# Kernel optimization log

Hardware: AMD Instinct MI355X
Metric: run time of the kernel (lower is better)

Reference implementation:

```python
import jax, jax.numpy as jnp
import numpy as np

B, D, H = 4096, 1024, 1024


def setup_inputs() -> dict:
    key = jax.random.key(0)
    ks = jax.random.split(key, 20)
    s_in = 1.0 / np.sqrt(D)
    s_hid = 1.0 / np.sqrt(H)
    inp = {
        "x_t": jax.random.normal(ks[0], (B, D), dtype=jnp.float32),
        "h_t_1": jax.random.normal(ks[1], (B, H), dtype=jnp.float32),
        "c_t_1": jax.random.normal(ks[2], (B, H), dtype=jnp.float32),
        # input-to-hidden weights (nn.Linear: y = x @ W.T + b), stacked i,f,o,z
        "W": jax.random.uniform(ks[3], (4, H, D), minval=-s_in, maxval=s_in, dtype=jnp.float32),
        "bW": jax.random.uniform(ks[4], (4, H), minval=-s_in, maxval=s_in, dtype=jnp.float32),
        # hidden-to-hidden weights, stacked i,f,o,z
        "U": jax.random.uniform(ks[5], (4, H, H), minval=-s_hid, maxval=s_hid, dtype=jnp.float32),
        "bU": jax.random.uniform(ks[6], (4, H), minval=-s_hid, maxval=s_hid, dtype=jnp.float32),
    }
    return inp


def reference(x_t, h_t_1, c_t_1, W, bW, U, bU):
    # Two stacked GEMMs: [B,D]x[4,H,D] -> [4,B,H], [B,H]x[4,H,H] -> [4,B,H]
    gx = jnp.einsum("bd,ghd->gbh", x_t, W) + bW[:, None, :]
    gh = jnp.einsum("bh,gkh->gbk", h_t_1, U) + bU[:, None, :]
    g = gx + gh  # [4, B, H] pre-activations for i, f, o, z
    i = jax.nn.sigmoid(g[0])
    f = jax.nn.sigmoid(g[1])
    o = jax.nn.sigmoid(g[2])
    z = jnp.tanh(g[3])
    c_t = i * z + f * c_t_1
    h_t = o * jnp.tanh(c_t)
    return (h_t, c_t)
```

## Files before the change

kernel.cpp:

```cpp
#include <hip/hip_runtime.h>
#include <math.h>

#define Mm 4096
#define Nn 4096
#define Kk 2048

typedef __bf16 bf16x8 __attribute__((ext_vector_type(8)));
typedef float f32x4 __attribute__((ext_vector_type(4)));

__device__ __forceinline__ unsigned short f2bf(float f) {
    union { float f; unsigned u; } v; v.f = f;
    unsigned r = v.u + 0x7FFFu + ((v.u >> 16) & 1u);
    return (unsigned short)(r >> 16);
}

__global__ void pack_bf16(const float* __restrict__ x, const float* __restrict__ h,
                          const float* __restrict__ W, const float* __restrict__ U,
                          const float* __restrict__ bW, const float* __restrict__ bU,
                          unsigned short* __restrict__ Xc, unsigned short* __restrict__ Wc,
                          float* __restrict__ bsum) {
    if (blockIdx.x == 0) {
#pragma unroll
        for (int j = 0; j < 16; ++j) {
            int n = threadIdx.x * 16 + j;
            int hh = n >> 2, g = n & 3;
            bsum[n] = bW[g * 1024 + hh] + bU[g * 1024 + hh];
        }
    }
    const int PER = (4096 * 1024) / 4;
    for (int t = blockIdx.x * blockDim.x + threadIdx.x; t < 4 * PER;
         t += gridDim.x * blockDim.x) {
        int region = t >> 20;
        int i = t & (PER - 1);
        int row = i >> 8;
        int c4  = i & 255;
        const float* src = (region == 0) ? x : (region == 1) ? h : (region == 2) ? W : U;
        float4 v = reinterpret_cast<const float4*>(src)[i];
        ushort4 o;
        o.x = f2bf(v.x); o.y = f2bf(v.y); o.z = f2bf(v.z); o.w = f2bf(v.w);
        if (region < 2) {
            *reinterpret_cast<ushort4*>(Xc + (size_t)row * 2048 + (region << 10) + c4 * 4) = o;
        } else {
            int g = row >> 10, hh = row & 1023;
            *reinterpret_cast<ushort4*>(Wc + (size_t)(hh * 4 + g) * 2048 + ((region & 1) << 10) + c4 * 4) = o;
        }
    }
}

__device__ __forceinline__ void gl16(const void* g, void* l) {
    __builtin_amdgcn_global_load_lds(
        (const __attribute__((address_space(1))) void*)g,
        (__attribute__((address_space(3))) void*)l, 16, 0, 0);
}

#define A_OFF(p, ah) (((p) * 2 + (ah)) * 16384)
#define B_OFF(p, hb) (65536 + ((p) * 2 + (hb)) * 16384)

__global__ __launch_bounds__(512, 2) void gemm_8ph(const unsigned short* __restrict__ A,
                                                   const unsigned short* __restrict__ Bw,
                                                   const float* __restrict__ bsum,
                                                   const float* __restrict__ cprev,
                                                   float* __restrict__ out) {
    extern __shared__ char lds[];
    const int tid = threadIdx.x, lane = tid & 63, wave = tid >> 6;
    const int wm = wave >> 2, wn = wave & 3;

    const int bid = blockIdx.x;
    const int swz = (bid & 7) * 32 + (bid >> 3);
    const int bm = swz & 15, bn = swz >> 4;
    const size_t Crow0 = (size_t)bm * 256, Ccol0 = (size_t)bn * 256;

    const int srow = wave * 8 + (lane >> 3);
    const int scolswz = (((lane & 7) ^ (lane >> 3)) << 4);
    const char* aS[2][2];
    const char* bS[2][2];
#pragma unroll
    for (int ah = 0; ah < 2; ++ah)
#pragma unroll
        for (int j = 0; j < 2; ++j) {
            aS[ah][j] = (const char*)A  + (size_t)(Crow0 + ah * 128 + j * 64 + srow) * 4096 + scolswz;
            bS[ah][j] = (const char*)Bw + (size_t)(Ccol0 + ah * 128 + j * 64 + srow) * 4096 + scolswz;
        }

#define STG_A(p, ah, kb) do { \
        gl16(aS[ah][0] + (kb), lds + A_OFF(p, ah) + wave * 1024); \
        gl16(aS[ah][1] + (kb), lds + A_OFF(p, ah) + 8192 + wave * 1024); } while (0)
#define STG_B(p, hb, kb) do { \
        gl16(bS[hb][0] + (kb), lds + B_OFF(p, hb) + wave * 1024); \
        gl16(bS[hb][1] + (kb), lds + B_OFF(p, hb) + 8192 + wave * 1024); } while (0)

    const int arowB = (wm * 64 + (lane & 15)) * 128;
    const int browB = ((wn & 1) * 64 + (lane & 15)) * 128;
    const int c0 = (((lane >> 4) << 4)) ^ ((lane & 7) << 4);
    const int c1 = (64 + ((lane >> 4) << 4)) ^ ((lane & 7) << 4);
    const int bhb = wn >> 1;

#define LDA(p, ah, mfl, ck) (*(const bf16x8*)(lds + A_OFF(p, ah) + arowB + (mfl) * 2048 + (ck)))
#define LDB(p, nf, ck)      (*(const bf16x8*)(lds + B_OFF(p, bhb) + browB + (nf) * 2048 + (ck)))

    f32x4 acc[2][4][4] = {};

#define MF8(ah, mf, ak0, ak1) \
    acc[ah][mf][0] = __builtin_amdgcn_mfma_f32_16x16x32_bf16(ak0, b00, acc[ah][mf][0], 0, 0, 0); \
    acc[ah][mf][0] = __builtin_amdgcn_mfma_f32_16x16x32_bf16(ak1, b01, acc[ah][mf][0], 0, 0, 0); \
    acc[ah][mf][1] = __builtin_amdgcn_mfma_f32_16x16x32_bf16(ak0, b10, acc[ah][mf][1], 0, 0, 0); \
    acc[ah][mf][1] = __builtin_amdgcn_mfma_f32_16x16x32_bf16(ak1, b11, acc[ah][mf][1], 0, 0, 0); \
    acc[ah][mf][2] = __builtin_amdgcn_mfma_f32_16x16x32_bf16(ak0, b20, acc[ah][mf][2], 0, 0, 0); \
    acc[ah][mf][2] = __builtin_amdgcn_mfma_f32_16x16x32_bf16(ak1, b21, acc[ah][mf][2], 0, 0, 0); \
    acc[ah][mf][3] = __builtin_amdgcn_mfma_f32_16x16x32_bf16(ak0, b30, acc[ah][mf][3], 0, 0, 0); \
    acc[ah][mf][3] = __builtin_amdgcn_mfma_f32_16x16x32_bf16(ak1, b31, acc[ah][mf][3], 0, 0, 0);

#define PH_TAIL \
    __builtin_amdgcn_s_barrier(); \
    asm volatile("s_waitcnt lgkmcnt(0)" ::: "memory"); \
    __builtin_amdgcn_s_setprio(1);

#define PH_END \
    __builtin_amdgcn_s_setprio(0); \
    __builtin_amdgcn_s_barrier();

#define GROUP(p, kbA1, kbT2) \
    { \
        bf16x8 b00 = LDB(p, 0, c0), b01 = LDB(p, 0, c1), b10 = LDB(p, 1, c0), b11 = LDB(p, 1, c1); \
        bf16x8 b20 = LDB(p, 2, c0), b21 = LDB(p, 2, c1), b30 = LDB(p, 3, c0), b31 = LDB(p, 3, c1); \
        {  \
            bf16x8 a00 = LDA(p, 0, 0, c0), a01 = LDA(p, 0, 0, c1); \
            bf16x8 a10 = LDA(p, 0, 1, c0), a11 = LDA(p, 0, 1, c1); \
            STG_A((p) ^ 1, 1, kbA1); \
            PH_TAIL MF8(0, 0, a00, a01) MF8(0, 1, a10, a11) PH_END \
        } \
        {  \
            bf16x8 a00 = LDA(p, 0, 2, c0), a01 = LDA(p, 0, 2, c1); \
            bf16x8 a10 = LDA(p, 0, 3, c0), a11 = LDA(p, 0, 3, c1); \
            STG_B(p, 0, kbT2); \
            PH_TAIL MF8(0, 2, a00, a01) MF8(0, 3, a10, a11) PH_END \
        } \
        {  \
            bf16x8 a00 = LDA(p, 1, 0, c0), a01 = LDA(p, 1, 0, c1); \
            bf16x8 a10 = LDA(p, 1, 1, c0), a11 = LDA(p, 1, 1, c1); \
            STG_A(p, 0, kbT2); \
            PH_TAIL MF8(1, 0, a00, a01) MF8(1, 1, a10, a11) PH_END \
        } \
        {  \
            bf16x8 a00 = LDA(p, 1, 2, c0), a01 = LDA(p, 1, 2, c1); \
            bf16x8 a10 = LDA(p, 1, 3, c0), a11 = LDA(p, 1, 3, c1); \
            STG_B(p, 1, kbT2); \
            __builtin_amdgcn_s_barrier(); \
            asm volatile("s_waitcnt lgkmcnt(0)" ::: "memory"); \
            __builtin_amdgcn_s_setprio(1); \
            MF8(1, 2, a00, a01) MF8(1, 3, a10, a11) \
            __builtin_amdgcn_s_setprio(0); \
            asm volatile("s_waitcnt vmcnt(6)" ::: "memory"); \
            __builtin_amdgcn_s_barrier(); \
        } \
    }

    STG_B(0, 0, 0);
    STG_A(0, 0, 0);
    STG_B(0, 1, 0);
    STG_A(0, 1, 0);
    STG_B(1, 0, 128);
    STG_A(1, 0, 128);
    STG_B(1, 1, 128);
    asm volatile("s_waitcnt vmcnt(6)" ::: "memory");
    __builtin_amdgcn_s_barrier();

    for (int it = 0; it < 16; ++it) {
        const int t0 = 2 * it;
        const size_t kA1_0 = (size_t)(t0 + 1) * 128;
        const size_t kT2_0 = (t0 + 2 <= 31) ? (size_t)(t0 + 2) * 128 : 0;
        const size_t kA1_1 = kT2_0;
        const size_t kT2_1 = (t0 + 3 <= 31) ? (size_t)(t0 + 3) * 128 : 0;
        GROUP(0, kA1_0, kT2_0)
        GROUP(1, kA1_1, kT2_1)
    }

    __syncthreads();

    const int Hbase = (int)(Ccol0 >> 2);
    const int ec = lane & 15, er0 = (lane >> 4) * 4;

#pragma unroll
    for (int ah = 0; ah < 2; ++ah) {
        if (ah) __syncthreads();
#pragma unroll
        for (int mf = 0; mf < 4; ++mf)
#pragma unroll
            for (int r = 0; r < 4; ++r) {
                const int lrow = wm * 64 + mf * 16 + er0 + r;
                const int sw = (lrow & 4) << 4;
#pragma unroll
                for (int nf = 0; nf < 4; ++nf) {
                    const int col = wn * 64 + nf * 16 + ec;
                    *(float*)(lds + lrow * 1024 + ((col * 4) ^ sw)) = acc[ah][mf][nf][r];
                }
            }
        __syncthreads();
#pragma unroll
        for (int i = 0; i < 16; ++i) {
            const int lrow = i * 8 + wave;
            const int sw = (lrow & 4) << 4;
            f32x4 g4 = *(const f32x4*)(lds + lrow * 1024 + ((lane * 16) ^ sw));
            f32x4 bs = *(const f32x4*)(bsum + (size_t)(Hbase + lane) * 4);
            const size_t bg = Crow0 + ah * 128 + lrow;
            const size_t oidx = bg * 1024 + Hbase + lane;
            float cp = cprev[oidx];
            float gi = g4[0] + bs[0], gf = g4[1] + bs[1];
            float go = g4[2] + bs[2], gz = g4[3] + bs[3];
            float iv = 1.f / (1.f + __expf(-gi));
            float fv = 1.f / (1.f + __expf(-gf));
            float ov = 1.f / (1.f + __expf(-go));
            float zv = tanhf(gz);
            float cc = fmaf(iv, zv, fv * cp);
            float hv = ov * tanhf(cc);
            out[oidx] = hv;
            out[(1 << 22) + oidx] = cc;
        }
    }
}

extern "C" void kernel_launch(void* const* d_in, const int* in_sizes, int n_in,
                              void* d_out, int out_size, void* d_ws, size_t ws_size,
                              hipStream_t stream) {
    const float* x  = (const float*)d_in[0];
    const float* h  = (const float*)d_in[1];
    const float* c  = (const float*)d_in[2];
    const float* W  = (const float*)d_in[3];
    const float* bW = (const float*)d_in[4];
    const float* U  = (const float*)d_in[5];
    const float* bU = (const float*)d_in[6];
    float* out = (float*)d_out;

    char* ws = (char*)d_ws;
    unsigned short* Xc = (unsigned short*)ws;
    unsigned short* Wc = (unsigned short*)(ws + ((size_t)16 << 20));
    float* bsum = (float*)(ws + ((size_t)32 << 20));

    (void)hipFuncSetAttribute((const void*)gemm_8ph,
                              hipFuncAttributeMaxDynamicSharedMemorySize, 131072);

    hipLaunchKernelGGL(pack_bf16, dim3(2048), dim3(256), 0, stream,
                       x, h, W, U, bW, bU, Xc, Wc, bsum);
    hipLaunchKernelGGL(gemm_8ph, dim3(256), dim3(512), 131072, stream,
                       Xc, Wc, bsum, c, out);
}
```

Measured before the change: 87.68 us.

## Switch GEMM inner loop to 32x32x16 MFMA and prefetch epilogue c_prev

Replaces the 16x16x32 bf16 MFMA tiling with 32x32x16 MFMA tiles. This changes the LDS fragment addressing, the accumulator layout (f32x16 per 32x32 tile) and the epilogue's scatter of accumulators into LDS. The larger instruction cuts the number of LDS fragment loads per FLOP and the MFMA issue count. The epilogue now loads c_prev and the bias vector into registers before the final barrier, overlapping those global reads with the LDS stage. The cost is higher register pressure from the 32 prefetched c_prev values on top of the larger accumulators.

Result: slower. 96.89 us (+10.5%).

```diff
diff --git a/kernel.cpp b/kernel.cpp
--- a/kernel.cpp
+++ b/kernel.cpp
@@ -7,6 +7,7 @@
 
 typedef __bf16 bf16x8 __attribute__((ext_vector_type(8)));
 typedef float f32x4 __attribute__((ext_vector_type(4)));
+typedef float f32x16 __attribute__((ext_vector_type(16)));
 
 __device__ __forceinline__ unsigned short f2bf(float f) {
     union { float f; unsigned u; } v; v.f = f;
@@ -89,26 +90,31 @@
         gl16(bS[hb][0] + (kb), lds + B_OFF(p, hb) + wave * 1024); \
         gl16(bS[hb][1] + (kb), lds + B_OFF(p, hb) + 8192 + wave * 1024); } while (0)
 
-    const int arowB = (wm * 64 + (lane & 15)) * 128;
-    const int browB = ((wn & 1) * 64 + (lane & 15)) * 128;
-    const int c0 = (((lane >> 4) << 4)) ^ ((lane & 7) << 4);
-    const int c1 = (64 + ((lane >> 4) << 4)) ^ ((lane & 7) << 4);
+    const int arowB = (wm * 64 + (lane & 31)) * 128;
+    const int browB = ((wn & 1) * 64 + (lane & 31)) * 128;
+    const int kl = (lane >> 5) << 4;
+    const int sx = (lane & 7) << 4;
+    const int cK0 = (0  + kl) ^ sx;
+    const int cK1 = (32 + kl) ^ sx;
+    const int cK2 = (64 + kl) ^ sx;
+    const int cK3 = (96 + kl) ^ sx;
     const int bhb = wn >> 1;
 
-#define LDA(p, ah, mfl, ck) (*(const bf16x8*)(lds + A_OFF(p, ah) + arowB + (mfl) * 2048 + (ck)))
-#define LDB(p, nf, ck)      (*(const bf16x8*)(lds + B_OFF(p, bhb) + browB + (nf) * 2048 + (ck)))
-
-    f32x4 acc[2][4][4] = {};
-
-#define MF8(ah, mf, ak0, ak1) \
-    acc[ah][mf][0] = __builtin_amdgcn_mfma_f32_16x16x32_bf16(ak0, b00, acc[ah][mf][0], 0, 0, 0); \
-    acc[ah][mf][0] = __builtin_amdgcn_mfma_f32_16x16x32_bf16(ak1, b01, acc[ah][mf][0], 0, 0, 0); \
-    acc[ah][mf][1] = __builtin_amdgcn_mfma_f32_16x16x32_bf16(ak0, b10, acc[ah][mf][1], 0, 0, 0); \
-    acc[ah][mf][1] = __builtin_amdgcn_mfma_f32_16x16x32_bf16(ak1, b11, acc[ah][mf][1], 0, 0, 0); \
-    acc[ah][mf][2] = __builtin_amdgcn_mfma_f32_16x16x32_bf16(ak0, b20, acc[ah][mf][2], 0, 0, 0); \
-    acc[ah][mf][2] = __builtin_amdgcn_mfma_f32_16x16x32_bf16(ak1, b21, acc[ah][mf][2], 0, 0, 0); \
-    acc[ah][mf][3] = __builtin_amdgcn_mfma_f32_16x16x32_bf16(ak0, b30, acc[ah][mf][3], 0, 0, 0); \
-    acc[ah][mf][3] = __builtin_amdgcn_mfma_f32_16x16x32_bf16(ak1, b31, acc[ah][mf][3], 0, 0, 0);
+#define LDA(p, ah, mt, ck) (*(const bf16x8*)(lds + A_OFF(p, ah) + arowB + (mt) * 4096 + (ck)))
+#define LDB(p, nt, ck)     (*(const bf16x8*)(lds + B_OFF(p, bhb) + browB + (nt) * 4096 + (ck)))
+
+    f32x16 acc[2][2][2] = {};
+
+#define MFMA32(a, b, c) __builtin_amdgcn_mfma_f32_32x32x16_bf16(a, b, c, 0, 0, 0)
+#define MF8(ah, mt, A0, A1, A2, A3) \
+    acc[ah][mt][0] = MFMA32(A0, b00, acc[ah][mt][0]); \
+    acc[ah][mt][1] = MFMA32(A0, b10, acc[ah][mt][1]); \
+    acc[ah][mt][0] = MFMA32(A1, b01, acc[ah][mt][0]); \
+    acc[ah][mt][1] = MFMA32(A1, b11, acc[ah][mt][1]); \
+    acc[ah][mt][0] = MFMA32(A2, b02, acc[ah][mt][0]); \
+    acc[ah][mt][1] = MFMA32(A2, b12, acc[ah][mt][1]); \
+    acc[ah][mt][0] = MFMA32(A3, b03, acc[ah][mt][0]); \
+    acc[ah][mt][1] = MFMA32(A3, b13, acc[ah][mt][1]);
 
 #define PH_TAIL \
     __builtin_amdgcn_s_barrier(); \
@@ -121,34 +127,30 @@
 
 #define GROUP(p, kbA1, kbT2) \
     { \
-        bf16x8 b00 = LDB(p, 0, c0), b01 = LDB(p, 0, c1), b10 = LDB(p, 1, c0), b11 = LDB(p, 1, c1); \
-        bf16x8 b20 = LDB(p, 2, c0), b21 = LDB(p, 2, c1), b30 = LDB(p, 3, c0), b31 = LDB(p, 3, c1); \
-        {  \
-            bf16x8 a00 = LDA(p, 0, 0, c0), a01 = LDA(p, 0, 0, c1); \
-            bf16x8 a10 = LDA(p, 0, 1, c0), a11 = LDA(p, 0, 1, c1); \
+        bf16x8 b00 = LDB(p, 0, cK0), b01 = LDB(p, 0, cK1), b02 = LDB(p, 0, cK2), b03 = LDB(p, 0, cK3); \
+        bf16x8 b10 = LDB(p, 1, cK0), b11 = LDB(p, 1, cK1), b12 = LDB(p, 1, cK2), b13 = LDB(p, 1, cK3); \
+        {  \
+            bf16x8 a0 = LDA(p, 0, 0, cK0), a1 = LDA(p, 0, 0, cK1), a2 = LDA(p, 0, 0, cK2), a3 = LDA(p, 0, 0, cK3); \
             STG_A((p) ^ 1, 1, kbA1); \
-            PH_TAIL MF8(0, 0, a00, a01) MF8(0, 1, a10, a11) PH_END \
-        } \
-        {  \
-            bf16x8 a00 = LDA(p, 0, 2, c0), a01 = LDA(p, 0, 2, c1); \
-            bf16x8 a10 = LDA(p, 0, 3, c0), a11 = LDA(p, 0, 3, c1); \
+            PH_TAIL MF8(0, 0, a0, a1, a2, a3) PH_END \
+        } \
+        {  \
+            bf16x8 a0 = LDA(p, 0, 1, cK0), a1 = LDA(p, 0, 1, cK1), a2 = LDA(p, 0, 1, cK2), a3 = LDA(p, 0, 1, cK3); \
             STG_B(p, 0, kbT2); \
-            PH_TAIL MF8(0, 2, a00, a01) MF8(0, 3, a10, a11) PH_END \
-        } \
-        {  \
-            bf16x8 a00 = LDA(p, 1, 0, c0), a01 = LDA(p, 1, 0, c1); \
-            bf16x8 a10 = LDA(p, 1, 1, c0), a11 = LDA(p, 1, 1, c1); \
+            PH_TAIL MF8(0, 1, a0, a1, a2, a3) PH_END \
+        } \
+        {  \
+            bf16x8 a0 = LDA(p, 1, 0, cK0), a1 = LDA(p, 1, 0, cK1), a2 = LDA(p, 1, 0, cK2), a3 = LDA(p, 1, 0, cK3); \
             STG_A(p, 0, kbT2); \
-            PH_TAIL MF8(1, 0, a00, a01) MF8(1, 1, a10, a11) PH_END \
-        } \
-        {  \
-            bf16x8 a00 = LDA(p, 1, 2, c0), a01 = LDA(p, 1, 2, c1); \
-            bf16x8 a10 = LDA(p, 1, 3, c0), a11 = LDA(p, 1, 3, c1); \
+            PH_TAIL MF8(1, 0, a0, a1, a2, a3) PH_END \
+        } \
+        {  \
+            bf16x8 a0 = LDA(p, 1, 1, cK0), a1 = LDA(p, 1, 1, cK1), a2 = LDA(p, 1, 1, cK2), a3 = LDA(p, 1, 1, cK3); \
             STG_B(p, 1, kbT2); \
             __builtin_amdgcn_s_barrier(); \
             asm volatile("s_waitcnt lgkmcnt(0)" ::: "memory"); \
             __builtin_amdgcn_s_setprio(1); \
-            MF8(1, 2, a00, a01) MF8(1, 3, a10, a11) \
+            MF8(1, 1, a0, a1, a2, a3) \
             __builtin_amdgcn_s_setprio(0); \
             asm volatile("s_waitcnt vmcnt(6)" ::: "memory"); \
             __builtin_amdgcn_s_barrier(); \
@@ -175,43 +177,47 @@
         GROUP(1, kA1_1, kT2_1)
     }
 
+    const int Hbase = (int)(Ccol0 >> 2);
+
+    float cp[2][16];
+#pragma unroll
+    for (int ah = 0; ah < 2; ++ah)
+#pragma unroll
+        for (int i = 0; i < 16; ++i)
+            cp[ah][i] = cprev[(Crow0 + ah * 128 + i * 8 + wave) * 1024 + Hbase + lane];
+    const f32x4 bs = *(const f32x4*)(bsum + (size_t)(Hbase + lane) * 4);
+
     __syncthreads();
-
-    const int Hbase = (int)(Ccol0 >> 2);
-    const int ec = lane & 15, er0 = (lane >> 4) * 4;
 
 #pragma unroll
     for (int ah = 0; ah < 2; ++ah) {
         if (ah) __syncthreads();
 #pragma unroll
-        for (int mf = 0; mf < 4; ++mf)
-#pragma unroll
-            for (int r = 0; r < 4; ++r) {
-                const int lrow = wm * 64 + mf * 16 + er0 + r;
-                const int sw = (lrow & 4) << 4;
-#pragma unroll
-                for (int nf = 0; nf < 4; ++nf) {
-                    const int col = wn * 64 + nf * 16 + ec;
-                    *(float*)(lds + lrow * 1024 + ((col * 4) ^ sw)) = acc[ah][mf][nf][r];
+        for (int mt = 0; mt < 2; ++mt)
+#pragma unroll
+            for (int nt = 0; nt < 2; ++nt)
+#pragma unroll
+                for (int r = 0; r < 16; ++r) {
+                    const int lrow = wm * 64 + mt * 32 + (r & 3) + 8 * (r >> 2) + 4 * (lane >> 5);
+                    const int col = wn * 64 + nt * 32 + (lane & 31);
+                    *(float*)(lds + lrow * 1024 + ((col * 4) ^ ((lrow & 4) << 4))) =
+                        acc[ah][mt][nt][r];
                 }
-            }
         __syncthreads();
 #pragma unroll
         for (int i = 0; i < 16; ++i) {
             const int lrow = i * 8 + wave;
             const int sw = (lrow & 4) << 4;
             f32x4 g4 = *(const f32x4*)(lds + lrow * 1024 + ((lane * 16) ^ sw));
-            f32x4 bs = *(const f32x4*)(bsum + (size_t)(Hbase + lane) * 4);
             const size_t bg = Crow0 + ah * 128 + lrow;
             const size_t oidx = bg * 1024 + Hbase + lane;
-            float cp = cprev[oidx];
             float gi = g4[0] + bs[0], gf = g4[1] + bs[1];
             float go = g4[2] + bs[2], gz = g4[3] + bs[3];
             float iv = 1.f / (1.f + __expf(-gi));
             float fv = 1.f / (1.f + __expf(-gf));
             float ov = 1.f / (1.f + __expf(-go));
             float zv = tanhf(gz);
-            float cc = fmaf(iv, zv, fv * cp);
+            float cc = fmaf(iv, zv, fv * cp[ah][i]);
             float hv = ov * tanhf(cc);
             out[oidx] = hv;
             out[(1 << 22) + oidx] = cc;
```
